# Performance work log

Hardware: AMD Instinct MI355X
Metric: run time of the kernel (lower is better)

## Reference

```python
import jax, jax.numpy as jnp
import numpy as np

B, ROI, T, H, F = 4, 90, 200, 3, 96
HID = 96  # spGNN hidden dim == input_dim; GRU hidden == output_dim
BN_EPS = 1e-5


def setup_inputs() -> dict:
    key = jax.random.key(0)
    ks = jax.random.split(key, 8)
    x = jax.random.normal(ks[0], (B, ROI, T, H, F), jnp.float32)
    av = jax.random.normal(ks[1], (B, ROI, T, H, ROI), jnp.float32)
    keep = (jax.random.uniform(ks[2], (B, ROI, T, H, ROI)) < 0.1).astype(jnp.float32)
    a = av * keep
    s = 0.1
    W1 = jax.random.normal(ks[3], (F, HID), jnp.float32) * s
    b1 = jnp.zeros((HID,), jnp.float32)
    g1 = jnp.ones((HID,), jnp.float32); be1 = jnp.zeros((HID,), jnp.float32)
    W2 = jax.random.normal(ks[4], (HID, F), jnp.float32) * s
    b2 = jnp.zeros((F,), jnp.float32)
    g2 = jnp.ones((F,), jnp.float32); be2 = jnp.zeros((F,), jnp.float32)
    eps = jnp.zeros((1, 1), jnp.float32)  # spGNN epsilon parameter
    Wih = jax.random.normal(ks[5], (ROI, 3 * HID, F), jnp.float32) * s
    Whh = jax.random.normal(ks[6], (ROI, 3 * HID, HID), jnp.float32) * s
    bih = jnp.zeros((ROI, 3 * HID), jnp.float32)
    bhh = jnp.zeros((ROI, 3 * HID), jnp.float32)
    return dict(x=x, a=a, eps=eps, W1=W1, b1=b1, g1=g1, be1=be1,
                W2=W2, b2=b2, g2=g2, be2=be2,
                Wih=Wih, Whh=Whh, bih=bih, bhh=bhh)


def _bn_eval(v, g, b):
    # BatchNorm1d in eval mode with init running stats (mean=0, var=1)
    return v * (g / jnp.sqrt(1.0 + BN_EPS)) + b


def _gru_one_roi(xseq, Wih, Whh, bih, bhh):
    # xseq: (N, T, F); torch GRU gate order: reset, update, new
    xp = jnp.einsum('ntf,gf->ntg', xseq, Wih) + bih  # (N, T, 3*HID)
    def step(h, xt):
        hp = h @ Whh.T + bhh
        xr, xz, xn = jnp.split(xt, 3, axis=-1)
        hr, hz, hn = jnp.split(hp, 3, axis=-1)
        r = jax.nn.sigmoid(xr + hr)
        z = jax.nn.sigmoid(xz + hz)
        n = jnp.tanh(xn + r * hn)
        h2 = (1.0 - z) * n + z * h
        return h2, h2
    h0 = jnp.zeros((xseq.shape[0], Whh.shape[1]), xseq.dtype)
    _, ys = jax.lax.scan(step, h0, jnp.swapaxes(xp, 0, 1))
    return jnp.swapaxes(ys, 0, 1)  # (N, T, HID)


def reference(x, a, eps, W1, b1, g1, be1, W2, b2, g2, be2, Wih, Whh, bih, bhh):
    b, roi, t, hb, f = x.shape
    # block-diagonal sparse mm == per-(b,t,h) masked dense matmul over roi
    xr = jnp.transpose(x, (0, 2, 3, 1, 4))                       # (b,T,H,roi,F)
    mask = (jnp.transpose(a, (0, 2, 3, 1, 4)) != 0).astype(x.dtype)  # ones at nonzeros
    agg = jnp.einsum('bthij,bthjf->bthif', mask, xr) + eps[0, 0] * xr
    v = agg.reshape(-1, f)                                       # (b*T*H*roi, F)
    h1 = jax.nn.elu(_bn_eval(v @ W1 + b1, g1, be1))
    h2 = jax.nn.elu(_bn_eval(h1 @ W2 + b2, g2, be2))
    h = h2.reshape(b, t, hb, roi, f)
    h = jnp.transpose(h, (0, 2, 3, 1, 4)).reshape(b * hb, roi, t, f)  # (bH, roi, T, F)
    h = jax.nn.relu(h)  # dropout: eval mode -> identity
    out = jax.vmap(_gru_one_roi, in_axes=(1, 0, 0, 0, 0), out_axes=1)(h, Wih, Whh, bih, bhh)
    out = out.reshape(b, hb, roi, t, -1)
    return jnp.transpose(out, (0, 2, 3, 1, 4))  # (b, roi, T, H, HID)
```

## Files before the change

### kernel.cpp

```cpp
#include <hip/hip_runtime.h>

#define B_  4
#define ROI 90
#define T_  200
#define H_  3
#define F_  96
#define G3  288
#define TB  4
#define APAD 104
#define ABUF (96 * APAD * 2)
#define SMEM_A (4 * ABUF)

typedef _Float16 f16x4 __attribute__((ext_vector_type(4)));
typedef _Float16 f16x8 __attribute__((ext_vector_type(8)));
typedef float    f32x4 __attribute__((ext_vector_type(4)));

__global__ __launch_bounds__(384, 3) void stageA(
    const float* __restrict__ x, const float* __restrict__ a,
    const float* __restrict__ eps,
    const float* __restrict__ W1, const float* __restrict__ b1,
    const float* __restrict__ g1, const float* __restrict__ be1,
    const float* __restrict__ W2, const float* __restrict__ b2,
    const float* __restrict__ g2, const float* __restrict__ be2,
    float* __restrict__ hbuf)
{
    extern __shared__ __align__(16) char smem[];
    _Float16* xT  = (_Float16*)(smem);
    _Float16* msk = (_Float16*)(smem + ABUF);
    _Float16* w1T = (_Float16*)(smem + 2 * ABUF);
    _Float16* agg = (_Float16*)(smem + 3 * ABUF);

    const int blk = blockIdx.x;
    const int bb  = blk / (T_ * H_);
    const int rem = blk % (T_ * H_);
    const int t   = rem / H_;
    const int hb  = rem % H_;
    const int tid = threadIdx.x;
    const int w    = tid >> 6;
    const int lane = tid & 63;
    const int l15  = lane & 15;
    const int hig  = lane >> 4;

    const float epsv = eps[0];

    for (int idx = tid; idx < 1692; idx += 384) {
        if (idx < 576) {
            const int f = idx / 6, c = idx % 6;
            xT[f * APAD + 90 + c] = (_Float16)0.f;
        } else if (idx < 1116) {
            const int k = idx - 576; const int i = k / 6, c = k % 6;
            msk[i * APAD + 90 + c] = (_Float16)0.f;
        } else {
            const int k = idx - 1116; const int i = 90 + k / 96, c = k % 96;
            msk[i * APAD + c] = (_Float16)0.f;
        }
    }
    for (int idx = tid; idx < ROI * 24; idx += 384) {
        const int j = idx / 24, c4 = idx % 24;
        const float4 v = *(const float4*)(x + ((((long)bb * ROI + j) * T_ + t) * H_ + hb) * F_ + c4 * 4);
        xT[(c4 * 4 + 0) * APAD + j] = (_Float16)v.x;
        xT[(c4 * 4 + 1) * APAD + j] = (_Float16)v.y;
        xT[(c4 * 4 + 2) * APAD + j] = (_Float16)v.z;
        xT[(c4 * 4 + 3) * APAD + j] = (_Float16)v.w;
    }
    for (int idx = tid; idx < ROI * ROI; idx += 384) {
        const int i = idx / ROI, j = idx % ROI;
        const float av = a[((((long)bb * ROI + i) * T_ + t) * H_ + hb) * ROI + j];
        msk[i * APAD + j] = (_Float16)(av != 0.0f ? 1.0f : 0.0f);
    }
    for (int idx = tid; idx < 96 * 96; idx += 384) {
        const int f = idx / 96, n = idx % 96;
        w1T[n * APAD + f] = (_Float16)W1[f * 96 + n];
    }
    __syncthreads();

    {
        f16x8 a1[3];
        #pragma unroll
        for (int kt = 0; kt < 3; kt++)
            a1[kt] = *(const f16x8*)&xT[(w * 16 + l15) * APAD + kt * 32 + hig * 8];
        const int f0 = w * 16 + hig * 4;
        #pragma unroll
        for (int nt = 0; nt < 6; nt++) {
            f32x4 d = { 0.f, 0.f, 0.f, 0.f };
            #pragma unroll
            for (int kt = 0; kt < 3; kt++) {
                const f16x8 b = *(const f16x8*)&msk[(nt * 16 + l15) * APAD + kt * 32 + hig * 8];
                d = __builtin_amdgcn_mfma_f32_16x16x32_f16(a1[kt], b, d, 0, 0, 0);
            }
            const int i = nt * 16 + l15;
            f16x4 o;
            #pragma unroll
            for (int q = 0; q < 4; q++)
                o[q] = (_Float16)(d[q] + epsv * (float)xT[(f0 + q) * APAD + i]);
            *(f16x4*)&agg[i * APAD + f0] = o;
        }
    }
    __syncthreads();

    for (int idx = tid; idx < 96 * 96; idx += 384) {
        const int n = idx / 96, f = idx % 96;
        msk[f * APAD + n] = (_Float16)W2[n * 96 + f];
    }
    {
        f16x8 a2[3];
        #pragma unroll
        for (int kt = 0; kt < 3; kt++)
            a2[kt] = *(const f16x8*)&w1T[(w * 16 + l15) * APAD + kt * 32 + hig * 8];
        const int n0 = w * 16 + hig * 4;
        const float4 bv = *(const float4*)(b1 + n0);
        const float4 gv = *(const float4*)(g1 + n0);
        const float4 ev = *(const float4*)(be1 + n0);
        const float rs = rsqrtf(1.0f + 1e-5f);
        #pragma unroll
        for (int nt = 0; nt < 6; nt++) {
            f32x4 d = { 0.f, 0.f, 0.f, 0.f };
            #pragma unroll
            for (int kt = 0; kt < 3; kt++) {
                const f16x8 b = *(const f16x8*)&agg[(nt * 16 + l15) * APAD + kt * 32 + hig * 8];
                d = __builtin_amdgcn_mfma_f32_16x16x32_f16(a2[kt], b, d, 0, 0, 0);
            }
            const int i = nt * 16 + l15;
            f16x4 o;
            #pragma unroll
            for (int q = 0; q < 4; q++) {
                float y = (d[q] + ((const float*)&bv)[q]) * (((const float*)&gv)[q] * rs)
                          + ((const float*)&ev)[q];
                y = y > 0.f ? y : expm1f(y);
                o[q] = (_Float16)y;
            }
            *(f16x4*)&xT[i * APAD + n0] = o;
        }
    }
    __syncthreads();

    {
        f16x8 a3[3];
        #pragma unroll
        for (int kt = 0; kt < 3; kt++)
            a3[kt] = *(const f16x8*)&msk[(w * 16 + l15) * APAD + kt * 32 + hig * 8];
        const int f0 = w * 16 + hig * 4;
        const float4 bv = *(const float4*)(b2 + f0);
        const float4 gv = *(const float4*)(g2 + f0);
        const float4 ev = *(const float4*)(be2 + f0);
        const float rs = rsqrtf(1.0f + 1e-5f);
        #pragma unroll
        for (int nt = 0; nt < 6; nt++) {
            f32x4 d = { 0.f, 0.f, 0.f, 0.f };
            #pragma unroll
            for (int kt = 0; kt < 3; kt++) {
                const f16x8 b = *(const f16x8*)&xT[(nt * 16 + l15) * APAD + kt * 32 + hig * 8];
                d = __builtin_amdgcn_mfma_f32_16x16x32_f16(a3[kt], b, d, 0, 0, 0);
            }
            const int i = nt * 16 + l15;
            if (i < ROI) {
                float4 o;
                #pragma unroll
                for (int q = 0; q < 4; q++) {
                    float y = (d[q] + ((const float*)&bv)[q]) * (((const float*)&gv)[q] * rs)
                              + ((const float*)&ev)[q];
                    ((float*)&o)[q] = fmaxf(y, 0.f);
                }
                *(float4*)(hbuf + ((((long)bb * ROI + i) * T_ + t) * H_ + hb) * 96 + f0) = o;
            }
        }
    }
}

__global__ __launch_bounds__(384, 1) void stageC(
    const float* __restrict__ Wih, const float* __restrict__ Whh,
    const float* __restrict__ bih, const float* __restrict__ bhh,
    float* __restrict__ io)
{
    __shared__ __align__(16) _Float16 xact[2][16][104];
    __shared__ __align__(16) _Float16 hact[2][16][104];

    const int r    = blockIdx.x;
    const int tid  = threadIdx.x;
    const int w    = tid >> 6;
    const int lane = tid & 63;
    const int j    = lane & 15;
    const int hi   = lane >> 4;
    const int k0   = w * 16 + hi * 4;

    const float* wb0 = Wih + (long)r * G3 * 96;
    const float* wb1 = Whh + (long)r * G3 * 96;
    f16x8 wf[2][3][3];
    #pragma unroll
    for (int m = 0; m < 2; m++)
        #pragma unroll
        for (int g = 0; g < 3; g++)
            #pragma unroll
            for (int kt = 0; kt < 3; kt++) {
                const float* src = (m ? wb1 : wb0)
                    + ((long)g * 96 + w * 16 + j) * 96 + kt * 32 + hi * 8;
                const float4 va = *(const float4*)src;
                const float4 vb = *(const float4*)(src + 4);
                f16x8 t = { (_Float16)va.x, (_Float16)va.y, (_Float16)va.z, (_Float16)va.w,
                            (_Float16)vb.x, (_Float16)vb.y, (_Float16)vb.z, (_Float16)vb.w };
                wf[m][g][kt] = t;
            }
    f32x4 bias[2][3];
    #pragma unroll
    for (int m = 0; m < 2; m++)
        #pragma unroll
        for (int g = 0; g < 3; g++) {
            const float* bsrc = (m ? bhh : bih) + (long)r * G3 + g * 96 + w * 16 + hi * 4;
            f32x4 t = { bsrc[0], bsrc[1], bsrc[2], bsrc[3] };
            bias[m][g] = t;
        }

    const bool owns = (j < 12);
    const int  bb   = (j < 12) ? j / 3 : 0;
    const int  hb   = (j < 12) ? j % 3 : 0;
    float* ioptr = io + ((((long)bb * ROI + r) * T_) * H_ + hb) * 96 + k0;
    const f32x4 zero4 = { 0.f, 0.f, 0.f, 0.f };

    f32x4 cur[TB], nxt[TB];
    #pragma unroll
    for (int jj = 0; jj < TB; jj++)
        cur[jj] = owns ? *(const f32x4*)(ioptr + jj * (H_ * 96)) : zero4;

    {
        f16x4 z4 = { (_Float16)0.f, (_Float16)0.f, (_Float16)0.f, (_Float16)0.f };
        *(f16x4*)&hact[0][j][k0] = z4;
        *(f16x4*)&hact[1][j][k0] = z4;
        *(f16x4*)&xact[1][j][k0] = z4;
        f16x4 x0 = { (_Float16)cur[0][0], (_Float16)cur[0][1],
                     (_Float16)cur[0][2], (_Float16)cur[0][3] };
        *(f16x4*)&xact[0][j][k0] = x0;
    }
    float hprev[4] = { 0.f, 0.f, 0.f, 0.f };
    __syncthreads();

    for (int tt = 0; tt < T_ / TB; tt++) {
        f32x4 out[TB];
        #pragma unroll
        for (int jj = 0; jj < TB; jj++) {
            if (jj == 0) {
                if (tt + 1 < T_ / TB) {
                    #pragma unroll
                    for (int p = 0; p < TB; p++)
                        nxt[p] = owns ? *(const f32x4*)(ioptr + ((tt + 1) * TB + p) * (H_ * 96))
                                      : zero4;
                } else {
                    #pragma unroll
                    for (int p = 0; p < TB; p++) nxt[p] = zero4;
                }
            }
            const int p = jj & 1;

            f32x4 d[2][3];
            #pragma unroll
            for (int m = 0; m < 2; m++)
                #pragma unroll
                for (int g = 0; g < 3; g++) d[m][g] = bias[m][g];
            #pragma unroll
            for (int kt = 0; kt < 3; kt++) {
                const f16x8 bx = *(const f16x8*)&xact[p][j][kt * 32 + hi * 8];
                const f16x8 bh = *(const f16x8*)&hact[p][j][kt * 32 + hi * 8];
                #pragma unroll
                for (int g = 0; g < 3; g++) {
                    d[0][g] = __builtin_amdgcn_mfma_f32_16x16x32_f16(wf[0][g][kt], bx, d[0][g], 0, 0, 0);
                    d[1][g] = __builtin_amdgcn_mfma_f32_16x16x32_f16(wf[1][g][kt], bh, d[1][g], 0, 0, 0);
                }
            }

            f16x4 hq;
            f32x4 ov;
            #pragma unroll
            for (int q = 0; q < 4; q++) {
                const float xr = d[0][0][q], xz = d[0][1][q], xn = d[0][2][q];
                const float hr = d[1][0][q], hz = d[1][1][q], hn = d[1][2][q];
                const float rg = 1.f / (1.f + __expf(-(xr + hr)));
                const float zg = 1.f / (1.f + __expf(-(xz + hz)));
                const float pre = xn + rg * hn;
                const float ng = 1.f - 2.f / (__expf(2.f * pre) + 1.f);
                const float hnew = (1.f - zg) * ng + zg * hprev[q];
                hprev[q] = hnew;
                ov[q] = hnew;
                hq[q] = (_Float16)hnew;
            }
            out[jj] = ov;
            *(f16x4*)&hact[1 - p][j][k0] = hq;
            const f32x4 xv = (jj + 1 < TB) ? cur[jj + 1] : nxt[0];
            f16x4 xq = { (_Float16)xv[0], (_Float16)xv[1],
                         (_Float16)xv[2], (_Float16)xv[3] };
            *(f16x4*)&xact[1 - p][j][k0] = xq;
            __syncthreads();
        }

        if (owns) {
            #pragma unroll
            for (int jj = 0; jj < TB; jj++)
                *(f32x4*)(ioptr + (tt * TB + jj) * (H_ * 96)) = out[jj];
        }
        #pragma unroll
        for (int p = 0; p < TB; p++) cur[p] = nxt[p];
    }
}

extern "C" void kernel_launch(void* const* d_in, const int* in_sizes, int n_in,
                              void* d_out, int out_size, void* d_ws, size_t ws_size,
                              hipStream_t stream) {
    (void)in_sizes; (void)n_in; (void)out_size; (void)d_ws; (void)ws_size;
    const float* x   = (const float*)d_in[0];
    const float* a   = (const float*)d_in[1];
    const float* eps = (const float*)d_in[2];
    const float* W1  = (const float*)d_in[3];
    const float* b1  = (const float*)d_in[4];
    const float* g1  = (const float*)d_in[5];
    const float* be1 = (const float*)d_in[6];
    const float* W2  = (const float*)d_in[7];
    const float* b2  = (const float*)d_in[8];
    const float* g2  = (const float*)d_in[9];
    const float* be2 = (const float*)d_in[10];
    const float* Wih = (const float*)d_in[11];
    const float* Whh = (const float*)d_in[12];
    const float* bih = (const float*)d_in[13];
    const float* bhh = (const float*)d_in[14];
    float* out = (float*)d_out;

    stageA<<<B_ * T_ * H_, 384, SMEM_A, stream>>>(x, a, eps, W1, b1, g1, be1,
                                                  W2, b2, g2, be2, out);
    stageC<<<ROI, 384, 0, stream>>>(Wih, Whh, bih, bhh, out);
}
```

Baseline: 565.5 us.

## Software-pipeline GRU input projection one step ahead and use a lighter barrier

Restructures the recurrent GRU kernel so the input-projection MFMAs for step t+1 are computed during step t, off the serial hidden-state chain. The x-activation buffer is primed two steps ahead and only the hidden-state MFMAs remain on the critical path. __syncthreads is replaced by an explicit lgkmcnt wait plus s_barrier. Each step's output is now stored immediately instead of batched per four steps. Launch bounds are raised to allow two blocks per CU, which tightens the register budget and risks spills with the weights held in registers.

```diff
diff --git a/kernel.cpp b/kernel.cpp
--- a/kernel.cpp
+++ b/kernel.cpp
@@ -14,6 +14,12 @@
 typedef _Float16 f16x4 __attribute__((ext_vector_type(4)));
 typedef _Float16 f16x8 __attribute__((ext_vector_type(8)));
 typedef float    f32x4 __attribute__((ext_vector_type(4)));
+
+#define BAR() do {                                            \
+    asm volatile("s_waitcnt lgkmcnt(0)" ::: "memory");        \
+    __builtin_amdgcn_s_barrier();                             \
+    asm volatile("" ::: "memory");                            \
+} while (0)
 
 __global__ __launch_bounds__(384, 3) void stageA(
     const float* __restrict__ x, const float* __restrict__ a,
@@ -167,7 +173,7 @@
     }
 }
 
-__global__ __launch_bounds__(384, 1) void stageC(
+__global__ __launch_bounds__(384, 2) void stageC(
     const float* __restrict__ Wih, const float* __restrict__ Whh,
     const float* __restrict__ bih, const float* __restrict__ bhh,
     float* __restrict__ io)
@@ -223,81 +229,91 @@
 
     {
         f16x4 z4 = { (_Float16)0.f, (_Float16)0.f, (_Float16)0.f, (_Float16)0.f };
-        *(f16x4*)&hact[0][j][k0] = z4;
         *(f16x4*)&hact[1][j][k0] = z4;
-        *(f16x4*)&xact[1][j][k0] = z4;
         f16x4 x0 = { (_Float16)cur[0][0], (_Float16)cur[0][1],
                      (_Float16)cur[0][2], (_Float16)cur[0][3] };
+        f16x4 x1 = { (_Float16)cur[1][0], (_Float16)cur[1][1],
+                     (_Float16)cur[1][2], (_Float16)cur[1][3] };
         *(f16x4*)&xact[0][j][k0] = x0;
+        *(f16x4*)&xact[1][j][k0] = x1;
     }
     float hprev[4] = { 0.f, 0.f, 0.f, 0.f };
-    __syncthreads();
+    BAR();
+
+    f32x4 xpa[3], xpb[3];
+    #pragma unroll
+    for (int g = 0; g < 3; g++) xpa[g] = bias[0][g];
+    #pragma unroll
+    for (int kt = 0; kt < 3; kt++) {
+        const f16x8 bx = *(const f16x8*)&xact[0][j][kt * 32 + hi * 8];
+        #pragma unroll
+        for (int g = 0; g < 3; g++)
+            xpa[g] = __builtin_amdgcn_mfma_f32_16x16x32_f16(wf[0][g][kt], bx, xpa[g], 0, 0, 0);
+    }
+
+#define GRU_STEP(XC, XN, RB, WB, XRB, XWB, XNEXTV, TGLOB)                        \
+    {                                                                            \
+                    \
+        _Pragma("unroll")                                                        \
+        for (int g = 0; g < 3; g++) XN[g] = bias[0][g];                          \
+        _Pragma("unroll")                                                        \
+        for (int kt = 0; kt < 3; kt++) {                                         \
+            const f16x8 bx = *(const f16x8*)&xact[XRB][j][kt * 32 + hi * 8];     \
+            _Pragma("unroll")                                                    \
+            for (int g = 0; g < 3; g++)                                          \
+                XN[g] = __builtin_amdgcn_mfma_f32_16x16x32_f16(wf[0][g][kt], bx, XN[g], 0, 0, 0); \
+        }                                                                        \
+                                                 \
+        f32x4 d0 = bias[1][0], d1 = bias[1][1], d2 = bias[1][2];                 \
+        _Pragma("unroll")                                                        \
+        for (int kt = 0; kt < 3; kt++) {                                         \
+            const f16x8 bh = *(const f16x8*)&hact[RB][j][kt * 32 + hi * 8];      \
+            d0 = __builtin_amdgcn_mfma_f32_16x16x32_f16(wf[1][0][kt], bh, d0, 0, 0, 0); \
+            d1 = __builtin_amdgcn_mfma_f32_16x16x32_f16(wf[1][1][kt], bh, d1, 0, 0, 0); \
+            d2 = __builtin_amdgcn_mfma_f32_16x16x32_f16(wf[1][2][kt], bh, d2, 0, 0, 0); \
+        }                                                                        \
+        f16x4 hq; f32x4 ov;                                                      \
+        _Pragma("unroll")                                                        \
+        for (int q = 0; q < 4; q++) {                                            \
+            const float xr = XC[0][q], xz = XC[1][q], xn = XC[2][q];             \
+            const float hr = d0[q], hz = d1[q], hn = d2[q];                      \
+            const float rg = 1.f / (1.f + __expf(-(xr + hr)));                   \
+            const float zg = 1.f / (1.f + __expf(-(xz + hz)));                   \
+            const float pre = xn + rg * hn;                                      \
+            const float ng = 1.f - 2.f / (__expf(2.f * pre) + 1.f);              \
+            const float hnew = (1.f - zg) * ng + zg * hprev[q];                  \
+            hprev[q] = hnew; ov[q] = hnew; hq[q] = (_Float16)hnew;               \
+        }                                                                        \
+        *(f16x4*)&hact[WB][j][k0] = hq;                                          \
+        {                                                                        \
+            const f32x4 xv = (XNEXTV);                                           \
+            f16x4 xq = { (_Float16)xv[0], (_Float16)xv[1],                       \
+                         (_Float16)xv[2], (_Float16)xv[3] };                     \
+            *(f16x4*)&xact[XWB][j][k0] = xq;                                     \
+        }                                                                        \
+        if (owns) *(f32x4*)(ioptr + (TGLOB) * (H_ * 96)) = ov;                   \
+        BAR();                                                                   \
+    }
 
     for (int tt = 0; tt < T_ / TB; tt++) {
-        f32x4 out[TB];
-        #pragma unroll
-        for (int jj = 0; jj < TB; jj++) {
-            if (jj == 0) {
-                if (tt + 1 < T_ / TB) {
-                    #pragma unroll
-                    for (int p = 0; p < TB; p++)
-                        nxt[p] = owns ? *(const f32x4*)(ioptr + ((tt + 1) * TB + p) * (H_ * 96))
-                                      : zero4;
-                } else {
-                    #pragma unroll
-                    for (int p = 0; p < TB; p++) nxt[p] = zero4;
-                }
-            }
-            const int p = jj & 1;
-
-            f32x4 d[2][3];
-            #pragma unroll
-            for (int m = 0; m < 2; m++)
-                #pragma unroll
-                for (int g = 0; g < 3; g++) d[m][g] = bias[m][g];
-            #pragma unroll
-            for (int kt = 0; kt < 3; kt++) {
-                const f16x8 bx = *(const f16x8*)&xact[p][j][kt * 32 + hi * 8];
-                const f16x8 bh = *(const f16x8*)&hact[p][j][kt * 32 + hi * 8];
-                #pragma unroll
-                for (int g = 0; g < 3; g++) {
-                    d[0][g] = __builtin_amdgcn_mfma_f32_16x16x32_f16(wf[0][g][kt], bx, d[0][g], 0, 0, 0);
-                    d[1][g] = __builtin_amdgcn_mfma_f32_16x16x32_f16(wf[1][g][kt], bh, d[1][g], 0, 0, 0);
-                }
-            }
-
-            f16x4 hq;
-            f32x4 ov;
-            #pragma unroll
-            for (int q = 0; q < 4; q++) {
-                const float xr = d[0][0][q], xz = d[0][1][q], xn = d[0][2][q];
-                const float hr = d[1][0][q], hz = d[1][1][q], hn = d[1][2][q];
-                const float rg = 1.f / (1.f + __expf(-(xr + hr)));
-                const float zg = 1.f / (1.f + __expf(-(xz + hz)));
-                const float pre = xn + rg * hn;
-                const float ng = 1.f - 2.f / (__expf(2.f * pre) + 1.f);
-                const float hnew = (1.f - zg) * ng + zg * hprev[q];
-                hprev[q] = hnew;
-                ov[q] = hnew;
-                hq[q] = (_Float16)hnew;
-            }
-            out[jj] = ov;
-            *(f16x4*)&hact[1 - p][j][k0] = hq;
-            const f32x4 xv = (jj + 1 < TB) ? cur[jj + 1] : nxt[0];
-            f16x4 xq = { (_Float16)xv[0], (_Float16)xv[1],
-                         (_Float16)xv[2], (_Float16)xv[3] };
-            *(f16x4*)&xact[1 - p][j][k0] = xq;
-            __syncthreads();
-        }
-
-        if (owns) {
-            #pragma unroll
-            for (int jj = 0; jj < TB; jj++)
-                *(f32x4*)(ioptr + (tt * TB + jj) * (H_ * 96)) = out[jj];
-        }
+        if (tt + 1 < T_ / TB) {
+            #pragma unroll
+            for (int p = 0; p < TB; p++)
+                nxt[p] = owns ? *(const f32x4*)(ioptr + ((tt + 1) * TB + p) * (H_ * 96))
+                              : zero4;
+        } else {
+            #pragma unroll
+            for (int p = 0; p < TB; p++) nxt[p] = zero4;
+        }
+        const int t0 = tt * TB;
+        GRU_STEP(xpa, xpb, 1, 0, 1, 0, cur[2], t0 + 0)
+        GRU_STEP(xpb, xpa, 0, 1, 0, 1, cur[3], t0 + 1)
+        GRU_STEP(xpa, xpb, 1, 0, 1, 0, nxt[0], t0 + 2)
+        GRU_STEP(xpb, xpa, 0, 1, 0, 1, nxt[1], t0 + 3)
         #pragma unroll
         for (int p = 0; p < TB; p++) cur[p] = nxt[p];
     }
+#undef GRU_STEP
 }
 
 extern "C" void kernel_launch(void* const* d_in, const int* in_sizes, int n_in,
```

New measurement: 524.7 us. 1.08x faster.
